# Performance work log

Hardware: AMD Instinct MI355X
Metric: run time of the kernel (lower is better)

Reference implementation:

```python
import jax, jax.numpy as jnp
import numpy as np

N_NODES = 50000
N_HOPS = 4
N_EDGES = 800000
NFEAT = 512
HIDDEN = 512
NCLASS = 128
ATT_HID = 64


def setup_inputs() -> dict:
    key = jax.random.key(0)
    ks = jax.random.split(key, 12)
    s = lambda *sh: 1.0 / np.sqrt(sh[0])
    inp = {}
    inp['x'] = jax.random.normal(ks[0], (N_NODES, NFEAT), dtype=jnp.float32)
    inp['W1'] = jax.random.normal(ks[1], (NFEAT, HIDDEN), dtype=jnp.float32) * s(NFEAT)
    inp['W2'] = jax.random.normal(ks[2], (HIDDEN, NCLASS), dtype=jnp.float32) * s(HIDDEN)
    inp['b2'] = jax.random.normal(ks[3], (NCLASS,), dtype=jnp.float32) * 0.01
    inp['Wg'] = jax.random.normal(ks[4], (NCLASS, NCLASS), dtype=jnp.float32) * s(NCLASS)
    inp['Wa'] = jax.random.normal(ks[5], (2 * NCLASS, ATT_HID), dtype=jnp.float32) * s(2 * NCLASS)
    inp['ba'] = jax.random.normal(ks[6], (ATT_HID,), dtype=jnp.float32) * 0.01
    inp['va'] = jax.random.normal(ks[7], (ATT_HID,), dtype=jnp.float32) * s(ATT_HID)
    inp['adj_values'] = jax.random.uniform(ks[8], (N_HOPS, N_EDGES), dtype=jnp.float32)
    inp['adj_indices'] = jax.random.randint(ks[9], (N_HOPS, 2, N_EDGES), 0, N_NODES, dtype=jnp.int32)
    inp['idx'] = jnp.arange(N_NODES, dtype=jnp.int32)
    return inp


def reference(x, W1, W2, b2, Wg, Wa, ba, va, adj_values, adj_indices, idx):
    # x: [N, nfeat] -> relu(linear1) -> linear2 : [N, C]
    z = jax.nn.relu(x @ W1) @ W2 + b2  # [N, C]
    anchor = z[idx]                    # [Na, C]
    na = idx.shape[0]
    n_hops = adj_indices.shape[0]
    embs = [anchor]
    for h in range(n_hops):  # fixed small structural loop over hops
        rows = adj_indices[h, 0]  # destination anchor row per edge
        cols = adj_indices[h, 1]  # source node per edge
        # sparse matmul: agg[r] = sum_e v_e * z[cols_e]  (LayerConvol)
        agg = jax.ops.segment_sum(adj_values[h][:, None] * z[cols], rows, num_segments=na)
        embs.append(agg @ Wg)  # [Na, C]
    seq = jnp.stack(embs, axis=1)  # [Na, H+1, C]
    # AttenMlp: additive attention of anchor query over hop embeddings
    q = jnp.broadcast_to(anchor[:, None, :], seq.shape)       # [Na, H+1, C]
    feat = jnp.concatenate([q, seq], axis=-1)                 # [Na, H+1, 2C]
    scores = jnp.tanh(feat @ Wa + ba) @ va                    # [Na, H+1]
    alpha = jax.nn.softmax(scores, axis=1)
    out = jnp.einsum('nh,nhc->nc', alpha, seq)                # [Na, C]
    return jax.nn.log_softmax(out, axis=1)
```

## Files before the change

kernel.cpp:

```cpp
#include <hip/hip_runtime.h>

#define NA    50000
#define NFEAT 512
#define HID   512
#define NC    128
#define AH    64
#define NE    800000
#define NHOP  4
#define NBUCK 196
#define CAPB  5120

typedef __bf16 bf16x8 __attribute__((ext_vector_type(8)));
typedef float  f32x4  __attribute__((ext_vector_type(4)));

__device__ __forceinline__ unsigned short f2bf(float f){
  union { float f; unsigned u; } a; a.f = f;
  return (unsigned short)((a.u + 0x7fffu + ((a.u >> 16) & 1u)) >> 16);
}
__device__ __forceinline__ float bf2f(unsigned short h){
  union { unsigned u; float f; } a; a.u = ((unsigned)h) << 16;
  return a.f;
}
__device__ __forceinline__ float uasf(unsigned u){
  union { unsigned u; float f; } a; a.u = u;
  return a.f;
}
__device__ __forceinline__ float tanh_fast(float x){
  x = fminf(15.f, fmaxf(-15.f, x));
  float e = __expf(2.f * x);
  return (e - 1.f) / (e + 1.f);
}

__device__ __forceinline__ void g2l16(const void* g, void* l){
  __builtin_amdgcn_global_load_lds(
      (const __attribute__((address_space(1))) void*)g,
      (__attribute__((address_space(3))) void*)l, 16, 0, 0);
}


__global__ void cast_x_kernel(const float* __restrict__ in, unsigned short* __restrict__ out, int n4){
  int i = blockIdx.x * 256 + threadIdx.x;
  if (i >= n4) return;
  float4 v = reinterpret_cast<const float4*>(in)[i];
  ushort4 o; o.x = f2bf(v.x); o.y = f2bf(v.y); o.z = f2bf(v.z); o.w = f2bf(v.w);
  reinterpret_cast<ushort4*>(out)[i] = o;
}

__global__ void transpose_cast_kernel(const float* __restrict__ in, unsigned short* __restrict__ out,
                                      int R, int N){
  int i = blockIdx.x * 256 + threadIdx.x;
  if (i >= R * N) return;
  int n = i / R, k = i - n * R;
  out[i] = f2bf(in[(size_t)k * N + n]);
}

__global__ void build_wa_kernel(const float* __restrict__ Wa, unsigned short* __restrict__ WaT){
  int i = blockIdx.x * 256 + threadIdx.x;
  if (i >= 128 * 128) return;
  int n = i >> 7, k = i & 127;
  float v = (n < 64) ? Wa[(size_t)k * AH + n] : Wa[(size_t)(128 + k) * AH + (n - 64)];
  WaT[i] = f2bf(v);
}

template<int OP>
__global__ __launch_bounds__(256) void gemm_bt(
    const unsigned short* __restrict__ A, const unsigned short* __restrict__ BT,
    float* __restrict__ Cf, unsigned short* __restrict__ Cb,
    const float* __restrict__ bias,
    int M, int N, int K, long long Abatch, long long Cbatch)
{
  __shared__ unsigned short As[128 * 32];
  __shared__ unsigned short Bs[128 * 32];
  const int tid = threadIdx.x;
  const int wave = tid >> 6, lane = tid & 63;
  A += (size_t)blockIdx.z * Abatch;
  const size_t coff = (size_t)blockIdx.z * Cbatch;
  const int row0 = blockIdx.x * 128, col0 = blockIdx.y * 128;
  const int wr = (wave >> 1) * 64, wc = (wave & 1) * 64;
  f32x4 acc[4][4];
  #pragma unroll
  for (int m = 0; m < 4; m++)
    #pragma unroll
    for (int n = 0; n < 4; n++) acc[m][n] = (f32x4){0.f, 0.f, 0.f, 0.f};
  const int lrow = lane >> 2, lk = (lane & 3) * 8;

  for (int k0 = 0; k0 < K; k0 += 32){
    __syncthreads();
    #pragma unroll
    for (int j = 0; j < 2; j++){
      const int rb = (wave * 2 + j) * 16;
      const int ra = rb + lrow;
      int gr = row0 + ra; gr = gr < M ? gr : M - 1;
      g2l16(A + (size_t)gr * K + k0 + lk, As + rb * 32);
      int gc = col0 + ra; gc = gc < N ? gc : N - 1;
      g2l16(BT + (size_t)gc * K + k0 + lk, Bs + rb * 32);
    }
    __syncthreads();
    bf16x8 af[4], bfr[4];
    #pragma unroll
    for (int m = 0; m < 4; m++)
      af[m] = *reinterpret_cast<const bf16x8*>(&As[(wr + m * 16 + (lane & 15)) * 32 + (lane >> 4) * 8]);
    #pragma unroll
    for (int n = 0; n < 4; n++)
      bfr[n] = *reinterpret_cast<const bf16x8*>(&Bs[(wc + n * 16 + (lane & 15)) * 32 + (lane >> 4) * 8]);
    #pragma unroll
    for (int m = 0; m < 4; m++)
      #pragma unroll
      for (int n = 0; n < 4; n++)
        acc[m][n] = __builtin_amdgcn_mfma_f32_16x16x32_bf16(af[m], bfr[n], acc[m][n], 0, 0, 0);
  }

  const int rbase = row0 + wr + (lane >> 4) * 4;
  const int cbase = col0 + wc + (lane & 15);
  #pragma unroll
  for (int m = 0; m < 4; m++){
    #pragma unroll
    for (int n = 0; n < 4; n++){
      const int col = cbase + n * 16;
      #pragma unroll
      for (int i = 0; i < 4; i++){
        const int row = rbase + m * 16 + i;
        if (row < M && col < N){
          float v = acc[m][n][i];
          if (OP == 0){ v = v > 0.f ? v : 0.f; Cb[coff + (size_t)row * N + col] = f2bf(v); }
          else if (OP == 1){
            v += bias[col];
            Cf[(size_t)row * N + col] = v;
            Cb[(size_t)row * N + col] = f2bf(v);
          }
          else if (OP == 2){ Cb[coff + (size_t)row * N + col] = f2bf(v); }
          else            { Cf[coff + (size_t)row * N + col] = v; }
        }
      }
    }
  }
}

__global__ __launch_bounds__(256) void binA_kernel(
    const int* __restrict__ adji, const float* __restrict__ adjv,
    int* __restrict__ fill, long long* __restrict__ binned)
{
  const int h = blockIdx.y, tid = threadIdx.x;
  const int e0 = blockIdx.x * 2048;
  __shared__ int lhist[NBUCK], lbase[NBUCK], lfill[NBUCK];
  for (int i = tid; i < NBUCK; i += 256){ lhist[i] = 0; lfill[i] = 0; }
  __syncthreads();
  int rr[8]; unsigned hh[8]; float vv[8];
  #pragma unroll
  for (int k = 0; k < 8; k++){
    int e = e0 + k * 256 + tid;
    bool ok = e < NE;
    int r = ok ? adji[(size_t)h * 2 * NE + e] : -1;
    int c = ok ? adji[(size_t)h * 2 * NE + NE + e] : 0;
    vv[k] = ok ? adjv[(size_t)h * NE + e] : 0.f;
    rr[k] = r;
    hh[k] = ((unsigned)(r & 255) << 17) | (unsigned)c;
    if (ok) atomicAdd(&lhist[r >> 8], 1);
  }
  __syncthreads();
  if (tid < NBUCK) lbase[tid] = atomicAdd(&fill[h * NBUCK + tid], lhist[tid]);
  __syncthreads();
  #pragma unroll
  for (int k = 0; k < 8; k++){
    if (rr[k] >= 0){
      int b = rr[k] >> 8;
      int p = lbase[b] + atomicAdd(&lfill[b], 1);
      if (p < CAPB)
        binned[((size_t)(h * NBUCK + b)) * CAPB + p] =
            ((long long)hh[k] << 32) | (unsigned)__float_as_int(vv[k]);
    }
  }
}

__global__ __launch_bounds__(1024) void bscan_kernel(const int* __restrict__ fill,
                                                     int* __restrict__ bbase, int* __restrict__ offs){
  __shared__ int tmp[1024];
  int tid = threadIdx.x;
  int v = (tid < NHOP * NBUCK) ? fill[tid] : 0;
  tmp[tid] = v; __syncthreads();
  for (int o = 1; o < 1024; o <<= 1){
    int t = (tid >= o) ? tmp[tid - o] : 0;
    __syncthreads();
    tmp[tid] += t;
    __syncthreads();
  }
  if (tid < NHOP * NBUCK) bbase[tid] = tmp[tid] - v;
  if (tid == 0) offs[NHOP * NA] = NHOP * NE;
}

__global__ __launch_bounds__(256) void binB_kernel(
    const int* __restrict__ fill, const int* __restrict__ bbase,
    const long long* __restrict__ binned,
    int* __restrict__ offs, long long* __restrict__ pvc)
{
  const int b = blockIdx.x, h = blockIdx.y, tid = threadIdx.x;
  const int hb = h * NBUCK + b;
  const int cnt = min(fill[hb], CAPB);
  const long long* src = binned + (size_t)hb * CAPB;
  const int gbase = bbase[hb];
  const int rowbase = b << 8;
  const int nrows = min(256, NA - rowbase);
  __shared__ long long sdata[CAPB];
  __shared__ int lhist[256], lpre[256], lfill2[256];
  lhist[tid] = 0; lfill2[tid] = 0;
  __syncthreads();
  for (int p = tid; p < cnt; p += 256)
    atomicAdd(&lhist[(unsigned)(src[p] >> 32) >> 17], 1);
  __syncthreads();
  int v = lhist[tid]; lpre[tid] = v; __syncthreads();
  for (int o = 1; o < 256; o <<= 1){
    int t = (tid >= o) ? lpre[tid - o] : 0;
    __syncthreads();
    lpre[tid] += t;
    __syncthreads();
  }
  int excl = lpre[tid] - v;
  if (tid < nrows) offs[h * NA + rowbase + tid] = gbase + excl;
  lpre[tid] = excl;
  __syncthreads();
  for (int p = tid; p < cnt; p += 256){
    long long rec = src[p];
    unsigned hi = (unsigned)(rec >> 32);
    int lr = hi >> 17;
    long long out = (rec & 0xffffffffLL) | ((long long)(hi & 0x1ffffu) << 32);
    int pos = lpre[lr] + atomicAdd(&lfill2[lr], 1);
    if (pos < CAPB) sdata[pos] = out;
    else            pvc[(size_t)gbase + pos] = out;
  }
  __syncthreads();
  for (int p = tid; p < cnt; p += 256)
    pvc[(size_t)gbase + p] = sdata[p];
}

#define GR 4
__global__ __launch_bounds__(256) void gather_kernel(
    const int* __restrict__ offs, const long long* __restrict__ pvc,
    const unsigned short* __restrict__ zbf, unsigned short* __restrict__ aggbf)
{
  const int h = blockIdx.y;
  const int w = threadIdx.x >> 6, lane = threadIdx.x & 63;
  const int row = blockIdx.x * GR + w;
  const int base = h * NA + row;
  const int s = offs[base], e = offs[base + 1];
  __shared__ alignas(16) long long srec[GR][64];
  const unsigned* z32 = (const unsigned*)zbf;
  const int4* sr2 = (const int4*)&srec[w][0];
  float a0 = 0.f, a1 = 0.f;
  for (int p0 = s; p0 < e; p0 += 64){
    long long r = 0;
    if (p0 + lane < e) r = __builtin_nontemporal_load(&pvc[p0 + lane]);
    srec[w][lane] = r;
    const int pairs = (min(64, e - p0) + 1) >> 1;
    #pragma unroll 2
    for (int jj = 0; jj < pairs; jj++){
      int4 rr = sr2[jj];
      float    v0 = uasf((unsigned)rr.x);
      unsigned c0 = (unsigned)rr.y;
      float    v1 = uasf((unsigned)rr.z);
      unsigned c1 = (unsigned)rr.w;
      unsigned z0 = z32[(c0 << 6) + lane];
      unsigned z1 = z32[(c1 << 6) + lane];
      a0 += v0 * uasf(z0 << 16);
      a1 += v0 * uasf(z0 & 0xffff0000u);
      a0 += v1 * uasf(z1 << 16);
      a1 += v1 * uasf(z1 & 0xffff0000u);
    }
  }
  ushort2 o; o.x = f2bf(a0); o.y = f2bf(a1);
  *reinterpret_cast<ushort2*>(aggbf + (size_t)base * NC + lane * 2) = o;
}

__global__ __launch_bounds__(256) void final_kernel(
    const float* __restrict__ z, const unsigned short* __restrict__ embs,
    const float* __restrict__ ZW, const unsigned short* __restrict__ EW,
    const float* __restrict__ ba, const float* __restrict__ va,
    const int* __restrict__ idx, float* __restrict__ out)
{
  int tid = threadIdx.x, wave = tid >> 6, lane = tid & 63;
  int n = blockIdx.x * 4 + wave;
  if (n >= NA) return;
  int an = idx[n];
  float qa = ZW[(size_t)an * NC + lane] + ba[lane];
  float vaj = va[lane];
  float sc[5];
  {
    float s0 = ZW[(size_t)an * NC + 64 + lane];
    float t = tanh_fast(qa + s0) * vaj;
    #pragma unroll
    for (int o = 32; o; o >>= 1) t += __shfl_xor(t, o);
    sc[0] = t;
  }
  #pragma unroll
  for (int h = 1; h < 5; h++){
    float sh = bf2f(EW[((size_t)(h - 1) * NA + n) * AH + lane]);
    float t = tanh_fast(qa + sh) * vaj;
    #pragma unroll
    for (int o = 32; o; o >>= 1) t += __shfl_xor(t, o);
    sc[h] = t;
  }
  float m = sc[0];
  #pragma unroll
  for (int h = 1; h < 5; h++) m = fmaxf(m, sc[h]);
  float al[5], den = 0.f;
  #pragma unroll
  for (int h = 0; h < 5; h++){ al[h] = __expf(sc[h] - m); den += al[h]; }
  float inv = 1.f / den;
  float o0 = al[0] * z[(size_t)an * NC + lane];
  float o1 = al[0] * z[(size_t)an * NC + 64 + lane];
  #pragma unroll
  for (int h = 1; h < 5; h++){
    o0 += al[h] * bf2f(embs[((size_t)(h - 1) * NA + n) * NC + lane]);
    o1 += al[h] * bf2f(embs[((size_t)(h - 1) * NA + n) * NC + 64 + lane]);
  }
  o0 *= inv; o1 *= inv;
  float mx = fmaxf(o0, o1);
  #pragma unroll
  for (int o = 32; o; o >>= 1) mx = fmaxf(mx, __shfl_xor(mx, o));
  float se = __expf(o0 - mx) + __expf(o1 - mx);
  #pragma unroll
  for (int o = 32; o; o >>= 1) se += __shfl_xor(se, o);
  float ls = __logf(se);
  out[(size_t)n * NC + lane]      = o0 - mx - ls;
  out[(size_t)n * NC + 64 + lane] = o1 - mx - ls;
}


extern "C" void kernel_launch(void* const* d_in, const int* in_sizes, int n_in,
                              void* d_out, int out_size, void* d_ws, size_t ws_size,
                              hipStream_t stream)
{
  const float* x    = (const float*)d_in[0];
  const float* W1   = (const float*)d_in[1];
  const float* W2   = (const float*)d_in[2];
  const float* b2   = (const float*)d_in[3];
  const float* Wg   = (const float*)d_in[4];
  const float* Wa   = (const float*)d_in[5];
  const float* ba   = (const float*)d_in[6];
  const float* va   = (const float*)d_in[7];
  const float* adjv = (const float*)d_in[8];
  const int*   adji = (const int*)d_in[9];
  const int*   idx  = (const int*)d_in[10];
  float* out = (float*)d_out;
  (void)in_sizes; (void)n_in; (void)out_size; (void)ws_size;

  char* w = (char*)d_ws;
  auto alloc = [&](size_t b) -> char* { char* p = w; w += (b + 255) & ~(size_t)255; return p; };
  unsigned short* Xbf  = (unsigned short*)alloc((size_t)NA * NFEAT * 2);
  unsigned short* Hbuf = (unsigned short*)alloc((size_t)NA * HID * 2);
  unsigned short* W1T  = (unsigned short*)alloc((size_t)HID * NFEAT * 2);
  unsigned short* W2T  = (unsigned short*)alloc((size_t)NC * HID * 2);
  unsigned short* WgT  = (unsigned short*)alloc((size_t)NC * NC * 2);
  unsigned short* WaT  = (unsigned short*)alloc((size_t)NC * NC * 2);
  float*          z    = (float*)alloc((size_t)NA * NC * 4);
  unsigned short* zbf  = (unsigned short*)alloc((size_t)NA * NC * 2);
  float*          ZW   = (float*)alloc((size_t)NA * NC * 4);
  int* fill  = (int*)alloc((size_t)NHOP * NBUCK * 4);
  int* bbase = (int*)alloc((size_t)NHOP * NBUCK * 4);
  int* offs  = (int*)alloc(((size_t)NHOP * NA + 1) * 4);
  long long* pvc = (long long*)alloc((size_t)NHOP * NE * 8);
  long long* binned = (long long*)Xbf;
  unsigned short* embs  = Xbf;
  unsigned short* aggbf = Hbuf;
  unsigned short* EW    = Hbuf;

  cast_x_kernel<<<dim3((NA * NFEAT / 4 + 255) / 256), 256, 0, stream>>>(x, Xbf, NA * NFEAT / 4);
  transpose_cast_kernel<<<dim3((NFEAT * HID + 255) / 256), 256, 0, stream>>>(W1, W1T, NFEAT, HID);
  transpose_cast_kernel<<<dim3((HID * NC + 255) / 256), 256, 0, stream>>>(W2, W2T, HID, NC);
  transpose_cast_kernel<<<dim3((NC * NC + 255) / 256), 256, 0, stream>>>(Wg, WgT, NC, NC);
  build_wa_kernel<<<dim3(64), 256, 0, stream>>>(Wa, WaT);

  gemm_bt<0><<<dim3(391, 4, 1), 256, 0, stream>>>(Xbf, W1T, nullptr, Hbuf, nullptr, NA, HID, NFEAT, 0, 0);
  gemm_bt<1><<<dim3(391, 1, 1), 256, 0, stream>>>(Hbuf, W2T, z, zbf, b2, NA, NC, HID, 0, 0);

  hipMemsetAsync(fill, 0, (size_t)NHOP * NBUCK * 4, stream);
  binA_kernel<<<dim3((NE + 2047) / 2048, NHOP), 256, 0, stream>>>(adji, adjv, fill, binned);
  bscan_kernel<<<dim3(1), 1024, 0, stream>>>(fill, bbase, offs);
  binB_kernel<<<dim3(NBUCK, NHOP), 256, 0, stream>>>(fill, bbase, binned, offs, pvc);

  gather_kernel<<<dim3(NA / GR, NHOP), 256, 0, stream>>>(offs, pvc, zbf, aggbf);
  gemm_bt<2><<<dim3(391, 1, NHOP), 256, 0, stream>>>(aggbf, WgT, nullptr, embs, nullptr,
                                                     NA, NC, NC, (long long)NA * NC, (long long)NA * NC);
  gemm_bt<3><<<dim3(391, 1, 1), 256, 0, stream>>>(zbf, WaT, ZW, nullptr, nullptr, NA, NC, NC, 0, 0);
  gemm_bt<2><<<dim3(391, 1, NHOP), 256, 0, stream>>>(embs, WaT + 64 * 128, nullptr, EW, nullptr,
                                                     NA, AH, NC, (long long)NA * NC, (long long)NA * AH);

  final_kernel<<<dim3(NA / 4), 256, 0, stream>>>(z, embs, ZW, EW, ba, va, idx, out);
}
```

Measured before the change: 373.7 us.

## Fuse x cast into GEMM1, precompute Wg·Wa product, merge post-gather GEMMs

Removes the separate fp32→bf16 cast of x: the first GEMM now loads fp32 x tiles into LDS and converts them to bf16 while building MFMA fragments. Wg and the second half of Wa are folded into one 128x64 matrix, so the EW projection reads the aggregated features directly instead of waiting for embs. The three post-gather GEMMs (embs, EW, ZW) are merged into one launch with 9 z-slices, and the gather loop keeps two accumulators and processes four edges per iteration for more memory-level parallelism. In exchange the first GEMM moves twice as many A bytes per tile and does per-element conversions in its inner loop, and EW rounds differently because the fused weight is rounded to bf16 once.

```diff
diff --git a/kernel.cpp b/kernel.cpp
--- a/kernel.cpp
+++ b/kernel.cpp
@@ -38,14 +38,6 @@
 }
 
 
-__global__ void cast_x_kernel(const float* __restrict__ in, unsigned short* __restrict__ out, int n4){
-  int i = blockIdx.x * 256 + threadIdx.x;
-  if (i >= n4) return;
-  float4 v = reinterpret_cast<const float4*>(in)[i];
-  ushort4 o; o.x = f2bf(v.x); o.y = f2bf(v.y); o.z = f2bf(v.z); o.w = f2bf(v.w);
-  reinterpret_cast<ushort4*>(out)[i] = o;
-}
-
 __global__ void transpose_cast_kernel(const float* __restrict__ in, unsigned short* __restrict__ out,
                                       int R, int N){
   int i = blockIdx.x * 256 + threadIdx.x;
@@ -62,18 +54,30 @@
   WaT[i] = f2bf(v);
 }
 
-template<int OP>
+__global__ void wfuse_kernel(const float* __restrict__ Wa, const float* __restrict__ Wg,
+                             unsigned short* __restrict__ WfuseT){
+  int i = blockIdx.x * 256 + threadIdx.x;
+  if (i >= 64 * 128) return;
+  int j = i >> 7, n = i & 127;
+  float s = 0.f;
+  for (int k = 0; k < 128; k++)
+    s += Wa[(size_t)(128 + k) * AH + j] * Wg[(size_t)n * 128 + k];
+  WfuseT[i] = f2bf(s);
+}
+
+template<int OP, int AF32>
 __global__ __launch_bounds__(256) void gemm_bt(
-    const unsigned short* __restrict__ A, const unsigned short* __restrict__ BT,
+    const void* __restrict__ Avoid, const unsigned short* __restrict__ BT,
     float* __restrict__ Cf, unsigned short* __restrict__ Cb,
     const float* __restrict__ bias,
     int M, int N, int K, long long Abatch, long long Cbatch)
 {
-  __shared__ unsigned short As[128 * 32];
+  __shared__ unsigned short As[AF32 ? 128 * 64 : 128 * 32];
   __shared__ unsigned short Bs[128 * 32];
   const int tid = threadIdx.x;
   const int wave = tid >> 6, lane = tid & 63;
-  A += (size_t)blockIdx.z * Abatch;
+  const unsigned short* A16 = (const unsigned short*)Avoid + (size_t)blockIdx.z * Abatch;
+  const float* A32 = (const float*)Avoid;
   const size_t coff = (size_t)blockIdx.z * Cbatch;
   const int row0 = blockIdx.x * 128, col0 = blockIdx.y * 128;
   const int wr = (wave >> 1) * 64, wc = (wave & 1) * 64;
@@ -82,32 +86,53 @@
   for (int m = 0; m < 4; m++)
     #pragma unroll
     for (int n = 0; n < 4; n++) acc[m][n] = (f32x4){0.f, 0.f, 0.f, 0.f};
-  const int lrow = lane >> 2, lk = (lane & 3) * 8;
 
   for (int k0 = 0; k0 < K; k0 += 32){
     __syncthreads();
-    #pragma unroll
-    for (int j = 0; j < 2; j++){
-      const int rb = (wave * 2 + j) * 16;
-      const int ra = rb + lrow;
-      int gr = row0 + ra; gr = gr < M ? gr : M - 1;
-      g2l16(A + (size_t)gr * K + k0 + lk, As + rb * 32);
-      int gc = col0 + ra; gc = gc < N ? gc : N - 1;
-      g2l16(BT + (size_t)gc * K + k0 + lk, Bs + rb * 32);
-    }
-    __syncthreads();
-    bf16x8 af[4], bfr[4];
-    #pragma unroll
-    for (int m = 0; m < 4; m++)
-      af[m] = *reinterpret_cast<const bf16x8*>(&As[(wr + m * 16 + (lane & 15)) * 32 + (lane >> 4) * 8]);
+    if (AF32){
+      #pragma unroll
+      for (int j = 0; j < 4; j++){
+        const int rb = (wave * 4 + j) * 8;
+        int gr = row0 + rb + (lane >> 3); gr = gr < M ? gr : M - 1;
+        g2l16(A32 + (size_t)gr * K + k0 + (lane & 7) * 4, (float*)As + rb * 32);
+      }
+      #pragma unroll
+      for (int j = 0; j < 2; j++){
+        const int rb = (wave * 2 + j) * 16;
+        int gc = col0 + rb + (lane >> 2); gc = gc < N ? gc : N - 1;
+        g2l16(BT + (size_t)gc * K + k0 + (lane & 3) * 8, Bs + rb * 32);
+      }
+    } else {
+      #pragma unroll
+      for (int j = 0; j < 2; j++){
+        const int rb = (wave * 2 + j) * 16;
+        int gr = row0 + rb + (lane >> 2); gr = gr < M ? gr : M - 1;
+        g2l16(A16 + (size_t)gr * K + k0 + (lane & 3) * 8, As + rb * 32);
+        int gc = col0 + rb + (lane >> 2); gc = gc < N ? gc : N - 1;
+        g2l16(BT + (size_t)gc * K + k0 + (lane & 3) * 8, Bs + rb * 32);
+      }
+    }
+    __syncthreads();
+    bf16x8 bfr[4];
     #pragma unroll
     for (int n = 0; n < 4; n++)
       bfr[n] = *reinterpret_cast<const bf16x8*>(&Bs[(wc + n * 16 + (lane & 15)) * 32 + (lane >> 4) * 8]);
     #pragma unroll
-    for (int m = 0; m < 4; m++)
+    for (int m = 0; m < 4; m++){
+      bf16x8 a;
+      if (AF32){
+        const float* Asf = (const float*)As;
+        const float4* fp = (const float4*)&Asf[(wr + m * 16 + (lane & 15)) * 32 + (lane >> 4) * 8];
+        float4 f0 = fp[0], f1 = fp[1];
+        a[0] = (__bf16)f0.x; a[1] = (__bf16)f0.y; a[2] = (__bf16)f0.z; a[3] = (__bf16)f0.w;
+        a[4] = (__bf16)f1.x; a[5] = (__bf16)f1.y; a[6] = (__bf16)f1.z; a[7] = (__bf16)f1.w;
+      } else {
+        a = *reinterpret_cast<const bf16x8*>(&As[(wr + m * 16 + (lane & 15)) * 32 + (lane >> 4) * 8]);
+      }
       #pragma unroll
       for (int n = 0; n < 4; n++)
-        acc[m][n] = __builtin_amdgcn_mfma_f32_16x16x32_bf16(af[m], bfr[n], acc[m][n], 0, 0, 0);
+        acc[m][n] = __builtin_amdgcn_mfma_f32_16x16x32_bf16(a, bfr[n], acc[m][n], 0, 0, 0);
+    }
   }
 
   const int rbase = row0 + wr + (lane >> 4) * 4;
@@ -123,13 +148,80 @@
         if (row < M && col < N){
           float v = acc[m][n][i];
           if (OP == 0){ v = v > 0.f ? v : 0.f; Cb[coff + (size_t)row * N + col] = f2bf(v); }
-          else if (OP == 1){
+          else {
             v += bias[col];
             Cf[(size_t)row * N + col] = v;
             Cb[(size_t)row * N + col] = f2bf(v);
           }
-          else if (OP == 2){ Cb[coff + (size_t)row * N + col] = f2bf(v); }
-          else            { Cf[coff + (size_t)row * N + col] = v; }
+        }
+      }
+    }
+  }
+}
+
+__global__ __launch_bounds__(256) void gemm_sweep(
+    const unsigned short* __restrict__ aggbf, const unsigned short* __restrict__ zbf,
+    const unsigned short* __restrict__ WgT, const unsigned short* __restrict__ WfuseT,
+    const unsigned short* __restrict__ WaT,
+    unsigned short* __restrict__ embs, unsigned short* __restrict__ EW, float* __restrict__ ZW)
+{
+  const int zi = blockIdx.z;
+  const unsigned short* A; const unsigned short* BT;
+  unsigned short* Cb = nullptr; float* Cf = nullptr; int N;
+  if (zi < 4)      { A = aggbf + (size_t)zi * NA * NC;       BT = WgT;    Cb = embs + (size_t)zi * NA * NC; N = 128; }
+  else if (zi < 8) { A = aggbf + (size_t)(zi - 4) * NA * NC; BT = WfuseT; Cb = EW + (size_t)(zi - 4) * NA * AH; N = 64; }
+  else             { A = zbf;                                BT = WaT;    Cf = ZW; N = 128; }
+
+  __shared__ unsigned short As[128 * 32];
+  __shared__ unsigned short Bs[128 * 32];
+  const int tid = threadIdx.x;
+  const int wave = tid >> 6, lane = tid & 63;
+  const int row0 = blockIdx.x * 128;
+  const int wr = (wave >> 1) * 64, wc = (wave & 1) * 64;
+  f32x4 acc[4][4];
+  #pragma unroll
+  for (int m = 0; m < 4; m++)
+    #pragma unroll
+    for (int n = 0; n < 4; n++) acc[m][n] = (f32x4){0.f, 0.f, 0.f, 0.f};
+
+  for (int k0 = 0; k0 < 128; k0 += 32){
+    __syncthreads();
+    #pragma unroll
+    for (int j = 0; j < 2; j++){
+      const int rb = (wave * 2 + j) * 16;
+      int gr = row0 + rb + (lane >> 2); gr = gr < NA ? gr : NA - 1;
+      g2l16(A + (size_t)gr * 128 + k0 + (lane & 3) * 8, As + rb * 32);
+      int gc = rb + (lane >> 2); gc = gc < N ? gc : N - 1;
+      g2l16(BT + (size_t)gc * 128 + k0 + (lane & 3) * 8, Bs + rb * 32);
+    }
+    __syncthreads();
+    bf16x8 bfr[4];
+    #pragma unroll
+    for (int n = 0; n < 4; n++)
+      bfr[n] = *reinterpret_cast<const bf16x8*>(&Bs[(wc + n * 16 + (lane & 15)) * 32 + (lane >> 4) * 8]);
+    #pragma unroll
+    for (int m = 0; m < 4; m++){
+      bf16x8 a = *reinterpret_cast<const bf16x8*>(&As[(wr + m * 16 + (lane & 15)) * 32 + (lane >> 4) * 8]);
+      #pragma unroll
+      for (int n = 0; n < 4; n++)
+        acc[m][n] = __builtin_amdgcn_mfma_f32_16x16x32_bf16(a, bfr[n], acc[m][n], 0, 0, 0);
+    }
+  }
+
+  const int rbase = row0 + wr + (lane >> 4) * 4;
+  const int cbase = wc + (lane & 15);
+  #pragma unroll
+  for (int m = 0; m < 4; m++){
+    #pragma unroll
+    for (int n = 0; n < 4; n++){
+      const int col = cbase + n * 16;
+      #pragma unroll
+      for (int i = 0; i < 4; i++){
+        const int row = rbase + m * 16 + i;
+        if (row < NA && col < N){
+          float v = acc[m][n][i];
+          if (Cf) Cf[(size_t)row * N + col] = v;
+          else    Cb[(size_t)row * N + col] = f2bf(v);
         }
       }
     }
@@ -245,28 +337,28 @@
   __shared__ alignas(16) long long srec[GR][64];
   const unsigned* z32 = (const unsigned*)zbf;
   const int4* sr2 = (const int4*)&srec[w][0];
-  float a0 = 0.f, a1 = 0.f;
+  float a0 = 0.f, a1 = 0.f, b0 = 0.f, b1 = 0.f;
   for (int p0 = s; p0 < e; p0 += 64){
     long long r = 0;
     if (p0 + lane < e) r = __builtin_nontemporal_load(&pvc[p0 + lane]);
     srec[w][lane] = r;
-    const int pairs = (min(64, e - p0) + 1) >> 1;
+    const int quads = (min(64, e - p0) + 3) >> 2;
     #pragma unroll 2
-    for (int jj = 0; jj < pairs; jj++){
-      int4 rr = sr2[jj];
-      float    v0 = uasf((unsigned)rr.x);
-      unsigned c0 = (unsigned)rr.y;
-      float    v1 = uasf((unsigned)rr.z);
-      unsigned c1 = (unsigned)rr.w;
-      unsigned z0 = z32[(c0 << 6) + lane];
-      unsigned z1 = z32[(c1 << 6) + lane];
-      a0 += v0 * uasf(z0 << 16);
-      a1 += v0 * uasf(z0 & 0xffff0000u);
-      a0 += v1 * uasf(z1 << 16);
-      a1 += v1 * uasf(z1 & 0xffff0000u);
-    }
-  }
-  ushort2 o; o.x = f2bf(a0); o.y = f2bf(a1);
+    for (int q = 0; q < quads; q++){
+      int4 ra = sr2[2 * q], rb = sr2[2 * q + 1];
+      unsigned z0 = z32[((unsigned)ra.y << 6) + lane];
+      unsigned z1 = z32[((unsigned)ra.w << 6) + lane];
+      unsigned z2 = z32[((unsigned)rb.y << 6) + lane];
+      unsigned z3 = z32[((unsigned)rb.w << 6) + lane];
+      float v0 = uasf((unsigned)ra.x), v1 = uasf((unsigned)ra.z);
+      float v2 = uasf((unsigned)rb.x), v3 = uasf((unsigned)rb.z);
+      a0 += v0 * uasf(z0 << 16); a1 += v0 * uasf(z0 & 0xffff0000u);
+      b0 += v1 * uasf(z1 << 16); b1 += v1 * uasf(z1 & 0xffff0000u);
+      a0 += v2 * uasf(z2 << 16); a1 += v2 * uasf(z2 & 0xffff0000u);
+      b0 += v3 * uasf(z3 << 16); b1 += v3 * uasf(z3 & 0xffff0000u);
+    }
+  }
+  ushort2 o; o.x = f2bf(a0 + b0); o.y = f2bf(a1 + b1);
   *reinterpret_cast<ushort2*>(aggbf + (size_t)base * NC + lane * 2) = o;
 }
 
@@ -345,12 +437,13 @@
 
   char* w = (char*)d_ws;
   auto alloc = [&](size_t b) -> char* { char* p = w; w += (b + 255) & ~(size_t)255; return p; };
-  unsigned short* Xbf  = (unsigned short*)alloc((size_t)NA * NFEAT * 2);
+  unsigned short* Scr1 = (unsigned short*)alloc((size_t)NA * NFEAT * 2);
   unsigned short* Hbuf = (unsigned short*)alloc((size_t)NA * HID * 2);
   unsigned short* W1T  = (unsigned short*)alloc((size_t)HID * NFEAT * 2);
   unsigned short* W2T  = (unsigned short*)alloc((size_t)NC * HID * 2);
   unsigned short* WgT  = (unsigned short*)alloc((size_t)NC * NC * 2);
   unsigned short* WaT  = (unsigned short*)alloc((size_t)NC * NC * 2);
+  unsigned short* WfuseT = (unsigned short*)alloc((size_t)AH * NC * 2);
   float*          z    = (float*)alloc((size_t)NA * NC * 4);
   unsigned short* zbf  = (unsigned short*)alloc((size_t)NA * NC * 2);
   float*          ZW   = (float*)alloc((size_t)NA * NC * 4);
@@ -358,19 +451,19 @@
   int* bbase = (int*)alloc((size_t)NHOP * NBUCK * 4);
   int* offs  = (int*)alloc(((size_t)NHOP * NA + 1) * 4);
   long long* pvc = (long long*)alloc((size_t)NHOP * NE * 8);
-  long long* binned = (long long*)Xbf;
-  unsigned short* embs  = Xbf;
+  long long* binned = (long long*)Scr1;
+  unsigned short* embs  = Scr1;
   unsigned short* aggbf = Hbuf;
-  unsigned short* EW    = Hbuf;
-
-  cast_x_kernel<<<dim3((NA * NFEAT / 4 + 255) / 256), 256, 0, stream>>>(x, Xbf, NA * NFEAT / 4);
+  unsigned short* EW    = (unsigned short*)pvc;
+
   transpose_cast_kernel<<<dim3((NFEAT * HID + 255) / 256), 256, 0, stream>>>(W1, W1T, NFEAT, HID);
   transpose_cast_kernel<<<dim3((HID * NC + 255) / 256), 256, 0, stream>>>(W2, W2T, HID, NC);
   transpose_cast_kernel<<<dim3((NC * NC + 255) / 256), 256, 0, stream>>>(Wg, WgT, NC, NC);
   build_wa_kernel<<<dim3(64), 256, 0, stream>>>(Wa, WaT);
-
-  gemm_bt<0><<<dim3(391, 4, 1), 256, 0, stream>>>(Xbf, W1T, nullptr, Hbuf, nullptr, NA, HID, NFEAT, 0, 0);
-  gemm_bt<1><<<dim3(391, 1, 1), 256, 0, stream>>>(Hbuf, W2T, z, zbf, b2, NA, NC, HID, 0, 0);
+  wfuse_kernel<<<dim3(32), 256, 0, stream>>>(Wa, Wg, WfuseT);
+
+  gemm_bt<0, 1><<<dim3(391, 4, 1), 256, 0, stream>>>(x, W1T, nullptr, Hbuf, nullptr, NA, HID, NFEAT, 0, 0);
+  gemm_bt<1, 0><<<dim3(391, 1, 1), 256, 0, stream>>>(Hbuf, W2T, z, zbf, b2, NA, NC, HID, 0, 0);
 
   hipMemsetAsync(fill, 0, (size_t)NHOP * NBUCK * 4, stream);
   binA_kernel<<<dim3((NE + 2047) / 2048, NHOP), 256, 0, stream>>>(adji, adjv, fill, binned);
@@ -378,11 +471,7 @@
   binB_kernel<<<dim3(NBUCK, NHOP), 256, 0, stream>>>(fill, bbase, binned, offs, pvc);
 
   gather_kernel<<<dim3(NA / GR, NHOP), 256, 0, stream>>>(offs, pvc, zbf, aggbf);
-  gemm_bt<2><<<dim3(391, 1, NHOP), 256, 0, stream>>>(aggbf, WgT, nullptr, embs, nullptr,
-                                                     NA, NC, NC, (long long)NA * NC, (long long)NA * NC);
-  gemm_bt<3><<<dim3(391, 1, 1), 256, 0, stream>>>(zbf, WaT, ZW, nullptr, nullptr, NA, NC, NC, 0, 0);
-  gemm_bt<2><<<dim3(391, 1, NHOP), 256, 0, stream>>>(embs, WaT + 64 * 128, nullptr, EW, nullptr,
-                                                     NA, AH, NC, (long long)NA * NC, (long long)NA * AH);
+  gemm_sweep<<<dim3(391, 1, 9), 256, 0, stream>>>(aggbf, zbf, WgT, WfuseT, WaT, embs, EW, ZW);
 
   final_kernel<<<dim3(NA / 4), 256, 0, stream>>>(z, embs, ZW, EW, ba, va, idx, out);
 }
```

Measured after the change: 446.3 us. 19.4% more time.
